# Optimization experiments

Hardware: AMD Instinct MI355X
Metric: run time of the kernel (lower is better)

Reference implementation:

```python
import jax, jax.numpy as jnp
import numpy as np

PATCH = 16
FMAP = 14  # 224 // 16, feature-map / mask resolution
BLUR_K = np.array([[1., 2., 1.], [2., 4., 2.], [1., 2., 1.]], dtype=np.float32) / 16.0  # pascal(3), normalized


def _conv(x, w, stride, pad):
    return jax.lax.conv_general_dilated(
        x, w, (stride, stride), [(pad, pad), (pad, pad)],
        dimension_numbers=("NCHW", "OIHW", "NCHW"))


def _max_blur_pool(x):
    # MaxBlurPool2D(kernel_size=3, stride=2, max_pool_size=2, ceil_mode=False):
    x = jax.lax.reduce_window(x, -jnp.inf, jax.lax.max,
                              (1, 1, 2, 2), (1, 1, 1, 1), "VALID")
    C = x.shape[1]
    kw = jnp.broadcast_to(jnp.asarray(BLUR_K, x.dtype), (C, 1, 3, 3))
    return jax.lax.conv_general_dilated(
        x, kw, (2, 2), [(1, 1), (1, 1)],
        dimension_numbers=("NCHW", "OIHW", "NCHW"), feature_group_count=C)


def _up(m, hw):
    # upsample [B,1,FMAP,FMAP] mask to spatial size hw via repeat_interleave
    f = hw // FMAP
    return jnp.repeat(jnp.repeat(m, f, axis=2), f, axis=3)


def reference(x, masks, w1, w2):
    B = x.shape[0]
    m = masks.reshape(B, 1, FMAP, FMAP).astype(x.dtype)  # fmap-level active mask
    x = x * _up(m, x.shape[2])                 # _apply_masks: zero masked 16x16 patches
    x = _conv(x, w1, 2, 3)                     # B,64,112,112
    x = jax.nn.relu(x * _up(m, x.shape[2]))    # SparK-style sparse conv: re-mask output
    x = _max_blur_pool(x)                      # B,64,56,56
    x = _conv(x, w2, 2, 3)                     # B,768,28,28
    x = jax.nn.relu(x * _up(m, x.shape[2]))    # re-mask output of second sparse conv
    x = _max_blur_pool(x)                      # B,768,14,14
    B_, C, H, W = x.shape
    return x.reshape(B_, C, H * W).transpose(0, 2, 1)  # b (h w) c -> [B,196,768]


def setup_inputs() -> dict:
    key = jax.random.key(0)
    k1, k2, k3, k4 = jax.random.split(key, 4)
    x = jax.random.normal(k1, (64, 3, 224, 224), jnp.float32)
    masks = jax.random.randint(k2, (64, 196), 0, 2).astype(bool)
    # kaiming_normal fan_in scaling as in init_weight
    w1 = jax.random.normal(k3, (64, 3, 7, 7), jnp.float32) * np.float32(np.sqrt(2.0 / (3 * 49)))
    w2 = jax.random.normal(k4, (768, 64, 7, 7), jnp.float32) * np.float32(np.sqrt(2.0 / (64 * 49)))
    return {"x": x, "masks": masks, "w1": w1, "w2": w2}
```

## Files before the change

kernel.cpp:

```cpp
#include <hip/hip_runtime.h>
#include <stdint.h>

typedef __attribute__((ext_vector_type(8))) short short8;
typedef __attribute__((ext_vector_type(4))) float f32x4;

#define DEVFN static __device__ __forceinline__

DEVFN float bf2f(uint16_t u) { union { uint32_t i; float f; } v; v.i = ((uint32_t)u) << 16; return v.f; }
DEVFN uint16_t f2bf(float f) {
  union { float f; uint32_t i; } v; v.f = f;
  uint32_t u = v.i;
  u += 0x7fffu + ((u >> 16) & 1u);
  return (uint16_t)(u >> 16);
}
DEVFN int imin(int a, int b) { return a < b ? a : b; }

DEVFN void gl_lds16(const void* g, void* l) {
  __builtin_amdgcn_global_load_lds(
      (__attribute__((address_space(1))) void*)(void*)g,
      (__attribute__((address_space(3))) void*)l, 16, 0, 0);
}

DEVFN f32x4 mfma16(short8 a, short8 b, f32x4 c) {
  return __builtin_amdgcn_mfma_f32_16x16x32_bf16(a, b, c, 0, 0, 0);
}

static constexpr size_t OFF_XP   = 0;
static constexpr size_t OFF_W1T  = 27557888;
static constexpr size_t OFF_W2T  = 27586560;
static constexpr size_t OFF_Y1   = 32403456;
static constexpr size_t OFF_P1   = 135163904;
static constexpr size_t OFF_Y2   = 166653952;
static constexpr size_t OFF_LIST = 243724288;
static constexpr size_t OFF_CNT  = 243774464;
static constexpr size_t WS_NEED  = 243774664;

__global__ __launch_bounds__(256) void k_count(const int* __restrict__ masks, int* __restrict__ cnts) {
  int b = blockIdx.x;
  int gid = b * 256 + threadIdx.x;
  unsigned long long m = __ballot(masks[gid] != 0);
  __shared__ int wsum[4];
  if ((threadIdx.x & 63) == 0) wsum[threadIdx.x >> 6] = __popcll(m);
  __syncthreads();
  if (threadIdx.x == 0) cnts[b] = wsum[0] + wsum[1] + wsum[2] + wsum[3];
}

__global__ __launch_bounds__(256) void k_emit(const int* __restrict__ masks, const int* __restrict__ cnts,
                                              int* __restrict__ list, int* __restrict__ total) {
  int b = blockIdx.x;
  int gid = b * 256 + threadIdx.x;
  int lane = threadIdx.x & 63, wave = threadIdx.x >> 6;
  int base = 0;
  for (int i = 0; i < b; ++i) base += cnts[i];
  bool f = masks[gid] != 0;
  unsigned long long m = __ballot(f);
  __shared__ int wcnt[4];
  if (lane == 0) wcnt[wave] = __popcll(m);
  __syncthreads();
  int woff = 0;
  for (int i = 0; i < wave; ++i) woff += wcnt[i];
  if (f) list[base + woff + __popcll(m & ((1ull << lane) - 1ull))] = gid;
  if (b == 48 && threadIdx.x == 0)
    *total = base + wcnt[0] + wcnt[1] + wcnt[2] + wcnt[3];
}

__global__ __launch_bounds__(256) void k_prep(const float* __restrict__ x, const int* __restrict__ masks,
                                              uint16_t* __restrict__ xp) {
  int gid = blockIdx.x * 256 + threadIdx.x;
  int b = gid / 53824;
  int rc = gid - b * 53824;
  int r2 = rc / 232;
  int c2 = rc - r2 * 232;
  int r = r2 - 3, c = c2 - 3;
  uint16_t o0 = 0, o1 = 0, o2 = 0;
  if ((unsigned)r < 224u && (unsigned)c < 224u) {
    if (masks[b * 196 + (r >> 4) * 14 + (c >> 4)]) {
      const float* px = x + (((size_t)b * 3) * 224 + r) * 224 + c;
      o0 = f2bf(px[0]);
      o1 = f2bf(px[50176]);
      o2 = f2bf(px[100352]);
    }
  }
  ushort4 o; o.x = o0; o.y = o1; o.z = o2; o.w = 0;
  *(ushort4*)(xp + (size_t)gid * 4) = o;
}

__global__ __launch_bounds__(256) void k_wt(const float* __restrict__ w1, const float* __restrict__ w2,
                                            uint16_t* __restrict__ w1t, uint16_t* __restrict__ w2t) {
  int gid = blockIdx.x * 256 + threadIdx.x;
  if (gid < 14336) {
    int kh = gid / 2048; int r = gid - kh * 2048;
    int oc = r >> 5, slot = r & 31;
    int kw = slot >> 2, ic = slot & 3;
    float v = 0.f;
    if (kw < 7 && ic < 3) v = w1[((oc * 3 + ic) * 7 + kh) * 7 + kw];
    w1t[gid] = f2bf(v);
  } else {
    int g2 = gid - 14336;
    int khw = g2 / 49152; int r = g2 - khw * 49152;
    int oc = r >> 6, ic = r & 63;
    int kh = khw / 7, kw = khw - kh * 7;
    w2t[g2] = f2bf(w2[((oc * 64 + ic) * 7 + kh) * 7 + kw]);
  }
}

__global__ __launch_bounds__(256, 3) void k_conv1(const uint16_t* __restrict__ xp, const uint16_t* __restrict__ w1t,
                                                  const int* __restrict__ list, const int* __restrict__ count,
                                                  uint16_t* __restrict__ y1) {
  __shared__ uint16_t sB[7 * 64 * 32];
  __shared__ int sc[2];

  int cnt = *count;
  int blk = blockIdx.x;
  if (blk * 2 >= cnt) return;
  int tid = threadIdx.x, lane = tid & 63, wave = tid >> 6;
  int csw = (lane & 3) ^ ((lane >> 2) & 3);

  {
    const char* wg = (const char*)w1t;
    char* wl = (char*)sB;
#pragma unroll
    for (int t = 0; t < 7; ++t) {
      int ldsoff = t * 4096 + wave * 1024;
      int goff = t * 4096 + (wave * 16 + (lane >> 2)) * 64 + csw * 16;
      gl_lds16(wg + goff, wl + ldsoff);
    }
  }
  if (tid < 2) sc[tid] = list[imin(blk * 2 + tid, cnt - 1)];
  __syncthreads();

  int wm = wave * 32, mrow = lane & 15, kg = lane >> 4;

  const uint16_t* baseA[2];
#pragma unroll
  for (int i = 0; i < 2; ++i) {
    int row = wm + 16 * i + mrow;
    int cell = sc[row >> 6];
    int b = cell / 196, cc = cell - b * 196;
    int ci = cc / 14, cj = cc - ci * 14;
    int p = row & 63;
    int oh = ci * 8 + (p >> 3), ow = cj * 8 + (p & 7);
    baseA[i] = xp + (((size_t)(b * 232 + 2 * oh)) * 232 + 2 * ow) * 4 + kg * 8;
  }
  int ksw = (kg ^ (mrow & 3)) * 8;

  f32x4 acc[2][4];
#pragma unroll
  for (int i = 0; i < 2; ++i)
#pragma unroll
    for (int j = 0; j < 4; ++j) acc[i][j] = f32x4{0.f, 0.f, 0.f, 0.f};

#pragma unroll
  for (int kh = 0; kh < 7; ++kh) {
    short8 a0 = *(const short8*)(baseA[0] + kh * 928);
    short8 a1 = *(const short8*)(baseA[1] + kh * 928);
    const uint16_t* Bk = sB + kh * 2048;
#pragma unroll
    for (int j = 0; j < 4; ++j) {
      short8 bj = *(const short8*)(Bk + (16 * j + mrow) * 32 + ksw);
      acc[0][j] = mfma16(a0, bj, acc[0][j]);
      acc[1][j] = mfma16(a1, bj, acc[1][j]);
    }
  }

#pragma unroll
  for (int i = 0; i < 2; ++i) {
    int rbase = wm + 16 * i;
    int cellidx = blk * 2 + (rbase >> 6);
    if (cellidx >= cnt) continue;
    int cell = sc[rbase >> 6];
    int b = cell / 196, cc = cell - b * 196;
    int ci = cc / 14, cj = cc - ci * 14;
#pragma unroll
    for (int j = 0; j < 4; ++j) {
      int oc = 16 * j + mrow;
#pragma unroll
      for (int r = 0; r < 4; ++r) {
        int row = rbase + kg * 4 + r;
        int p = row & 63;
        int oh = ci * 8 + (p >> 3), ow = cj * 8 + (p & 7);
        float v = acc[i][j][r];
        v = v > 0.f ? v : 0.f;
        y1[(((size_t)(b * 112 + oh)) * 112 + ow) * 64 + oc] = f2bf(v);
      }
    }
  }
}

__global__ __launch_bounds__(256) void k_pool1(const uint16_t* __restrict__ y1, const int* __restrict__ masks,
                                               uint16_t* __restrict__ p1) {
  __shared__ uint16_t sY[18 * 18 * 64];
  int b = blockIdx.y;
  int tile = blockIdx.x;
  int tr = tile >> 3, tc = tile & 7;
  int pr0 = tr * 8, pc0 = tc * 8;
  int R0 = 2 * pr0 - 7, C0 = 2 * pc0 - 7;
  int tid = threadIdx.x;
  const int* mb = masks + b * 196;

  for (int idx = tid; idx < 2592; idx += 256) {
    int pix = idx >> 3, ch = idx & 7;
    int pr = pix / 18, pc = pix - pr * 18;
    int r = R0 + pr, c = C0 + pc;
    short8 v = {0, 0, 0, 0, 0, 0, 0, 0};
    if ((unsigned)r < 112u && (unsigned)c < 112u && mb[(r >> 3) * 14 + (c >> 3)])
      v = *(const short8*)(y1 + (((size_t)(b * 112 + r)) * 112 + c) * 64 + ch * 8);
    *(short8*)(sY + ((size_t)(pr * 18 + pc)) * 64 + ch * 8) = v;
  }
  __syncthreads();

  for (int it = tid; it < 512; it += 256) {
    int opix = it >> 3, ch = it & 7;
    int lr = opix >> 3, lc = opix & 7;
    int pr = pr0 + lr, pc = pc0 + lc;
    if (pr >= 62 || pc >= 62) continue;
    int oh = pr - 3, ow = pc - 3;
    float acc[8] = {0.f, 0.f, 0.f, 0.f, 0.f, 0.f, 0.f, 0.f};
    if ((unsigned)oh < 56u && (unsigned)ow < 56u) {
      float hm_prev[3][8];
#pragma unroll
      for (int dd = 0; dd < 4; ++dd) {
        float yv[4][8];
        const uint16_t* src = sY + ((size_t)((2 * lr + dd) * 18 + 2 * lc)) * 64 + ch * 8;
#pragma unroll
        for (int e = 0; e < 4; ++e) {
          short8 t8 = *(const short8*)(src + e * 64);
#pragma unroll
          for (int k = 0; k < 8; ++k) yv[e][k] = bf2f((uint16_t)t8[k]);
        }
        float hm[3][8];
#pragma unroll
        for (int e = 0; e < 3; ++e) {
          int qc = 2 * ow - 1 + e;
          float cv = ((unsigned)qc <= 110u) ? 1.f : 0.f;
#pragma unroll
          for (int k = 0; k < 8; ++k) hm[e][k] = cv * fmaxf(yv[e][k], yv[e + 1][k]);
        }
        if (dd > 0) {
          int d = dd - 1;
          int qr = 2 * oh - 1 + d;
          if ((unsigned)qr <= 110u) {
            float wd = (d == 1) ? 2.f : 1.f;
#pragma unroll
            for (int e = 0; e < 3; ++e) {
              float w = wd * ((e == 1) ? 2.f : 1.f);
#pragma unroll
              for (int k = 0; k < 8; ++k) acc[k] += w * fmaxf(hm_prev[e][k], hm[e][k]);
            }
          }
        }
#pragma unroll
        for (int e = 0; e < 3; ++e)
#pragma unroll
          for (int k = 0; k < 8; ++k) hm_prev[e][k] = hm[e][k];
      }
#pragma unroll
      for (int k = 0; k < 8; ++k) acc[k] *= (1.f / 16.f);
    }
    short8 o;
#pragma unroll
    for (int k = 0; k < 8; ++k) o[k] = (short)f2bf(acc[k]);
    *(short8*)(p1 + (((size_t)(b * 62 + pr)) * 62 + pc) * 64 + ch * 8) = o;
  }
}

__global__ __launch_bounds__(256, 3) void k_conv2(const uint16_t* __restrict__ p1, const uint16_t* __restrict__ w2t,
                                                  const int* __restrict__ list, const int* __restrict__ count,
                                                  uint16_t* __restrict__ y2) {
  __shared__ uint16_t sA[128 * 64];
  __shared__ uint16_t sBt[128 * 64];
  __shared__ int scs[32];

  int cnt = *count;
  int gx = blockIdx.x;
  int xcd = gx & 7, s = gx >> 3;
  int y = s % 6, mtl = s / 6;
  int mt = xcd + 8 * mtl;
  if (mt * 32 >= cnt) return;
  int ocb = y * 128;
  int tid = threadIdx.x, lane = tid & 63, wave = tid >> 6;
  int csw = (lane & 7) ^ ((lane >> 3) & 7);

  if (tid < 32) scs[tid] = list[imin(mt * 32 + tid, cnt - 1)];
  __syncthreads();

  int qm = wave & 1, qn = wave >> 1;
  int mrow = lane & 15, kg = lane >> 4;

  const char* gA[4];
#pragma unroll
  for (int t = 0; t < 4; ++t) {
    int r = wave * 32 + t * 8 + (lane >> 3);
    int cell = scs[r >> 2];
    int b = cell / 196, cc = cell - b * 196;
    int ci = cc / 14, cj = cc - ci * 14;
    int p = r & 3;
    int oh = 2 * ci + (p >> 1), ow = 2 * cj + (p & 1);
    gA[t] = (const char*)p1 + (((size_t)(b * 62 + 2 * oh)) * 62 + 2 * ow) * 128 + csw * 16;
  }
  const char* gB[4];
#pragma unroll
  for (int t = 0; t < 4; ++t) {
    int oc = ocb + wave * 32 + t * 8 + (lane >> 3);
    gB[t] = (const char*)w2t + (size_t)oc * 128 + csw * 16;
  }

  f32x4 acc[4][4];
#pragma unroll
  for (int i = 0; i < 4; ++i)
#pragma unroll
    for (int j = 0; j < 4; ++j) acc[i][j] = f32x4{0.f, 0.f, 0.f, 0.f};

  int sw8 = mrow & 7;
  int kh = 0, kw = 0;
  char* la = (char*)sA + wave * 4096;
  char* lb = (char*)sBt + wave * 4096;
  int k0 = (kg ^ sw8) * 8;
  int k1 = ((4 + kg) ^ sw8) * 8;

#pragma unroll 1
  for (int it = 0; it < 49; ++it) {
    size_t offA = (size_t)(kh * 62 + kw) * 128;
    size_t offB = (size_t)it * 98304;
#pragma unroll
    for (int t = 0; t < 4; ++t) gl_lds16(gA[t] + offA, la + t * 1024);
#pragma unroll
    for (int t = 0; t < 4; ++t) gl_lds16(gB[t] + offB, lb + t * 1024);
    __syncthreads();
    short8 a0[4], b0[4], a1[4], b1[4];
#pragma unroll
    for (int i = 0; i < 4; ++i)
      a0[i] = *(const short8*)(sA + (qm * 64 + 16 * i + mrow) * 64 + k0);
#pragma unroll
    for (int j = 0; j < 4; ++j)
      b0[j] = *(const short8*)(sBt + (qn * 64 + 16 * j + mrow) * 64 + k0);
#pragma unroll
    for (int i = 0; i < 4; ++i)
      a1[i] = *(const short8*)(sA + (qm * 64 + 16 * i + mrow) * 64 + k1);
#pragma unroll
    for (int j = 0; j < 4; ++j)
      b1[j] = *(const short8*)(sBt + (qn * 64 + 16 * j + mrow) * 64 + k1);
    __builtin_amdgcn_sched_barrier(0);
    __builtin_amdgcn_s_setprio(1);
#pragma unroll
    for (int i = 0; i < 4; ++i)
#pragma unroll
      for (int j = 0; j < 4; ++j)
        acc[i][j] = mfma16(a0[i], b0[j], acc[i][j]);
    __builtin_amdgcn_s_setprio(0);
    __builtin_amdgcn_sched_barrier(0);
    __builtin_amdgcn_s_setprio(1);
#pragma unroll
    for (int i = 0; i < 4; ++i)
#pragma unroll
      for (int j = 0; j < 4; ++j)
        acc[i][j] = mfma16(a1[i], b1[j], acc[i][j]);
    __builtin_amdgcn_s_setprio(0);
    __syncthreads();
    if (++kw == 7) { kw = 0; ++kh; }
  }

#pragma unroll
  for (int i = 0; i < 4; ++i) {
    int cellslot = qm * 16 + 4 * i + kg;
    int cellidx = mt * 32 + cellslot;
    if (cellidx >= cnt) continue;
    int cell = scs[cellslot];
    int b = cell / 196, cc = cell - b * 196;
    int ci = cc / 14, cj = cc - ci * 14;
#pragma unroll
    for (int j = 0; j < 4; ++j) {
      int oc = ocb + qn * 64 + 16 * j + mrow;
#pragma unroll
      for (int r = 0; r < 4; ++r) {
        int oh = 2 * ci + (r >> 1), ow = 2 * cj + (r & 1);
        float v = acc[i][j][r];
        v = v > 0.f ? v : 0.f;
        y2[(((size_t)(b * 784)) + oh * 28 + ow) * 768 + oc] = f2bf(v);
      }
    }
  }
}

__global__ __launch_bounds__(256) void k_pool2(const uint16_t* __restrict__ y2, const int* __restrict__ masks,
                                               float* __restrict__ out) {
  __shared__ uint16_t sY[4 * 28 * 128];
  int chunk = blockIdx.x, pi = blockIdx.y, b = blockIdx.z;
  int ch0 = chunk * 128;
  int tid = threadIdx.x;
  const int* mb = masks + b * 196;

  for (int idx = tid; idx < 1792; idx += 256) {
    int rc = idx >> 4;
    int sub = idx & 15;
    int k = rc / 28, c = rc - k * 28;
    int r = 2 * pi - 1 + k;
    short8 v = {0, 0, 0, 0, 0, 0, 0, 0};
    if ((unsigned)r < 28u && mb[(r >> 1) * 14 + (c >> 1)])
      v = *(const short8*)(y2 + (((size_t)(b * 784)) + r * 28 + c) * 768 + ch0 + sub * 8);
    *(short8*)(sY + ((size_t)(k * 28 + c)) * 128 + sub * 8) = v;
  }
  __syncthreads();

  for (int idx = tid; idx < 1792; idx += 256) {
    int pj = idx >> 7, ch = idx & 127;
    float v[4][4];
#pragma unroll
    for (int e = 0; e < 4; ++e) {
      int col = 2 * pj - 1 + e;
      bool cv = (unsigned)col < 28u;
#pragma unroll
      for (int k = 0; k < 4; ++k)
        v[k][e] = cv ? bf2f(sY[((size_t)(k * 28 + col)) * 128 + ch]) : 0.f;
    }
    float acc = 0.f;
#pragma unroll
    for (int d = 0; d < 3; ++d) {
      int q = 2 * pi - 1 + d;
      float gd = ((unsigned)q <= 26u) ? ((d == 1) ? 2.f : 1.f) : 0.f;
      float s = 0.f;
#pragma unroll
      for (int e = 0; e < 3; ++e) {
        int q2 = 2 * pj - 1 + e;
        float ge = ((unsigned)q2 <= 26u) ? ((e == 1) ? 2.f : 1.f) : 0.f;
        float m = fmaxf(fmaxf(v[d][e], v[d + 1][e]), fmaxf(v[d][e + 1], v[d + 1][e + 1]));
        s += ge * m;
      }
      acc += gd * s;
    }
    out[(((size_t)(b * 196)) + pi * 14 + pj) * 768 + ch0 + ch] = acc * (1.f / 16.f);
  }
}

extern "C" void kernel_launch(void* const* d_in, const int* in_sizes, int n_in,
                              void* d_out, int out_size, void* d_ws, size_t ws_size,
                              hipStream_t stream) {
  const float* x     = (const float*)d_in[0];
  const int*   masks = (const int*)d_in[1];
  const float* w1    = (const float*)d_in[2];
  const float* w2    = (const float*)d_in[3];

  char* ws = (char*)d_ws;
  if (ws_size < WS_NEED) return;

  uint16_t* xp  = (uint16_t*)(ws + OFF_XP);
  uint16_t* w1t = (uint16_t*)(ws + OFF_W1T);
  uint16_t* w2t = (uint16_t*)(ws + OFF_W2T);
  uint16_t* y1  = (uint16_t*)(ws + OFF_Y1);
  uint16_t* p1  = (uint16_t*)(ws + OFF_P1);
  uint16_t* y2  = (uint16_t*)(ws + OFF_Y2);
  int* list     = (int*)(ws + OFF_LIST);
  int* cnts     = (int*)(ws + OFF_CNT);
  int* total    = cnts + 49;

  k_count<<<49, 256, 0, stream>>>(masks, cnts);
  k_emit<<<49, 256, 0, stream>>>(masks, cnts, list, total);
  k_prep<<<13456, 256, 0, stream>>>(x, masks, xp);
  k_wt<<<9464, 256, 0, stream>>>(w1, w2, w1t, w2t);
  k_conv1<<<6272, 256, 0, stream>>>(xp, w1t, list, total, y1);
  k_pool1<<<dim3(64, 64), 256, 0, stream>>>(y1, masks, p1);
  k_conv2<<<2352, 256, 0, stream>>>(p1, w2t, list, total, y2);
  k_pool2<<<dim3(6, 14, 64), 256, 0, stream>>>(y2, masks, (float*)d_out);
}
```

Baseline: 364.0 us.

## Double-buffer conv2 LDS tiles to overlap global loads with MFMA

```diff
diff --git a/kernel.cpp b/kernel.cpp
--- a/kernel.cpp
+++ b/kernel.cpp
@@ -264,11 +264,11 @@
   }
 }
 
-__global__ __launch_bounds__(256, 3) void k_conv2(const uint16_t* __restrict__ p1, const uint16_t* __restrict__ w2t,
+__global__ __launch_bounds__(256, 2) void k_conv2(const uint16_t* __restrict__ p1, const uint16_t* __restrict__ w2t,
                                                   const int* __restrict__ list, const int* __restrict__ count,
                                                   uint16_t* __restrict__ y2) {
-  __shared__ uint16_t sA[128 * 64];
-  __shared__ uint16_t sBt[128 * 64];
+  __shared__ uint16_t sA[2][128 * 64];
+  __shared__ uint16_t sBt[2][128 * 64];
   __shared__ int scs[32];
 
   int cnt = *count;
@@ -312,34 +312,47 @@
     for (int j = 0; j < 4; ++j) acc[i][j] = f32x4{0.f, 0.f, 0.f, 0.f};
 
   int sw8 = mrow & 7;
-  int kh = 0, kw = 0;
-  char* la = (char*)sA + wave * 4096;
-  char* lb = (char*)sBt + wave * 4096;
   int k0 = (kg ^ sw8) * 8;
   int k1 = ((4 + kg) ^ sw8) * 8;
+  int aoff = (qm * 64 + mrow) * 64;
+  int boff = (qn * 64 + mrow) * 64;
+
+  char* laA[2] = { (char*)sA[0] + wave * 4096, (char*)sA[1] + wave * 4096 };
+  char* laB[2] = { (char*)sBt[0] + wave * 4096, (char*)sBt[1] + wave * 4096 };
+
+#pragma unroll
+  for (int t = 0; t < 4; ++t) gl_lds16(gA[t], laA[0] + t * 1024);
+#pragma unroll
+  for (int t = 0; t < 4; ++t) gl_lds16(gB[t] + 0, laB[0] + t * 1024);
+  __syncthreads();
+
+  int kwn = 1, khn = 0;
+  int cur = 0;
 
 #pragma unroll 1
   for (int it = 0; it < 49; ++it) {
-    size_t offA = (size_t)(kh * 62 + kw) * 128;
-    size_t offB = (size_t)it * 98304;
-#pragma unroll
-    for (int t = 0; t < 4; ++t) gl_lds16(gA[t] + offA, la + t * 1024);
-#pragma unroll
-    for (int t = 0; t < 4; ++t) gl_lds16(gB[t] + offB, lb + t * 1024);
-    __syncthreads();
+    if (it < 48) {
+      size_t offA = (size_t)(khn * 62 + kwn) * 128;
+      size_t offB = (size_t)(it + 1) * 98304;
+      char* la = laA[cur ^ 1];
+      char* lb = laB[cur ^ 1];
+#pragma unroll
+      for (int t = 0; t < 4; ++t) gl_lds16(gA[t] + offA, la + t * 1024);
+#pragma unroll
+      for (int t = 0; t < 4; ++t) gl_lds16(gB[t] + offB, lb + t * 1024);
+      if (++kwn == 7) { kwn = 0; ++khn; }
+    }
+    const uint16_t* cA = sA[cur];
+    const uint16_t* cB = sBt[cur];
     short8 a0[4], b0[4], a1[4], b1[4];
 #pragma unroll
-    for (int i = 0; i < 4; ++i)
-      a0[i] = *(const short8*)(sA + (qm * 64 + 16 * i + mrow) * 64 + k0);
-#pragma unroll
-    for (int j = 0; j < 4; ++j)
-      b0[j] = *(const short8*)(sBt + (qn * 64 + 16 * j + mrow) * 64 + k0);
-#pragma unroll
-    for (int i = 0; i < 4; ++i)
-      a1[i] = *(const short8*)(sA + (qm * 64 + 16 * i + mrow) * 64 + k1);
-#pragma unroll
-    for (int j = 0; j < 4; ++j)
-      b1[j] = *(const short8*)(sBt + (qn * 64 + 16 * j + mrow) * 64 + k1);
+    for (int i = 0; i < 4; ++i) a0[i] = *(const short8*)(cA + aoff + 1024 * i + k0);
+#pragma unroll
+    for (int j = 0; j < 4; ++j) b0[j] = *(const short8*)(cB + boff + 1024 * j + k0);
+#pragma unroll
+    for (int i = 0; i < 4; ++i) a1[i] = *(const short8*)(cA + aoff + 1024 * i + k1);
+#pragma unroll
+    for (int j = 0; j < 4; ++j) b1[j] = *(const short8*)(cB + boff + 1024 * j + k1);
     __builtin_amdgcn_sched_barrier(0);
     __builtin_amdgcn_s_setprio(1);
 #pragma unroll
@@ -356,8 +369,12 @@
       for (int j = 0; j < 4; ++j)
         acc[i][j] = mfma16(a1[i], b1[j], acc[i][j]);
     __builtin_amdgcn_s_setprio(0);
-    __syncthreads();
-    if (++kw == 7) { kw = 0; ++kh; }
+    __builtin_amdgcn_sched_barrier(0);
+    asm volatile("s_waitcnt vmcnt(0)" ::: "memory");
+    __builtin_amdgcn_sched_barrier(0);
+    __builtin_amdgcn_s_barrier();
+    __builtin_amdgcn_sched_barrier(0);
+    cur ^= 1;
   }
 
 #pragma unroll
```

New measurement: 375.2 us. 1.03x slower.

## Fuse front-end prep kernels into one launch and vectorize pool2 epilogue

Applied to the files above, without the earlier changes.

```diff
diff --git a/kernel.cpp b/kernel.cpp
--- a/kernel.cpp
+++ b/kernel.cpp
@@ -35,72 +35,70 @@
 static constexpr size_t OFF_CNT  = 243774464;
 static constexpr size_t WS_NEED  = 243774664;
 
-__global__ __launch_bounds__(256) void k_count(const int* __restrict__ masks, int* __restrict__ cnts) {
-  int b = blockIdx.x;
-  int gid = b * 256 + threadIdx.x;
-  unsigned long long m = __ballot(masks[gid] != 0);
-  __shared__ int wsum[4];
-  if ((threadIdx.x & 63) == 0) wsum[threadIdx.x >> 6] = __popcll(m);
-  __syncthreads();
-  if (threadIdx.x == 0) cnts[b] = wsum[0] + wsum[1] + wsum[2] + wsum[3];
-}
-
-__global__ __launch_bounds__(256) void k_emit(const int* __restrict__ masks, const int* __restrict__ cnts,
-                                              int* __restrict__ list, int* __restrict__ total) {
-  int b = blockIdx.x;
-  int gid = b * 256 + threadIdx.x;
-  int lane = threadIdx.x & 63, wave = threadIdx.x >> 6;
-  int base = 0;
-  for (int i = 0; i < b; ++i) base += cnts[i];
-  bool f = masks[gid] != 0;
-  unsigned long long m = __ballot(f);
-  __shared__ int wcnt[4];
-  if (lane == 0) wcnt[wave] = __popcll(m);
-  __syncthreads();
-  int woff = 0;
-  for (int i = 0; i < wave; ++i) woff += wcnt[i];
-  if (f) list[base + woff + __popcll(m & ((1ull << lane) - 1ull))] = gid;
-  if (b == 48 && threadIdx.x == 0)
-    *total = base + wcnt[0] + wcnt[1] + wcnt[2] + wcnt[3];
-}
-
-__global__ __launch_bounds__(256) void k_prep(const float* __restrict__ x, const int* __restrict__ masks,
-                                              uint16_t* __restrict__ xp) {
-  int gid = blockIdx.x * 256 + threadIdx.x;
-  int b = gid / 53824;
-  int rc = gid - b * 53824;
-  int r2 = rc / 232;
-  int c2 = rc - r2 * 232;
-  int r = r2 - 3, c = c2 - 3;
-  uint16_t o0 = 0, o1 = 0, o2 = 0;
-  if ((unsigned)r < 224u && (unsigned)c < 224u) {
-    if (masks[b * 196 + (r >> 4) * 14 + (c >> 4)]) {
-      const float* px = x + (((size_t)b * 3) * 224 + r) * 224 + c;
-      o0 = f2bf(px[0]);
-      o1 = f2bf(px[50176]);
-      o2 = f2bf(px[100352]);
-    }
-  }
-  ushort4 o; o.x = o0; o.y = o1; o.z = o2; o.w = 0;
-  *(ushort4*)(xp + (size_t)gid * 4) = o;
-}
-
-__global__ __launch_bounds__(256) void k_wt(const float* __restrict__ w1, const float* __restrict__ w2,
-                                            uint16_t* __restrict__ w1t, uint16_t* __restrict__ w2t) {
-  int gid = blockIdx.x * 256 + threadIdx.x;
-  if (gid < 14336) {
-    int kh = gid / 2048; int r = gid - kh * 2048;
-    int oc = r >> 5, slot = r & 31;
-    int kw = slot >> 2, ic = slot & 3;
-    float v = 0.f;
-    if (kw < 7 && ic < 3) v = w1[((oc * 3 + ic) * 7 + kh) * 7 + kw];
-    w1t[gid] = f2bf(v);
+__global__ __launch_bounds__(256) void k_front(const int* __restrict__ masks, const float* __restrict__ x,
+                                               const float* __restrict__ w1, const float* __restrict__ w2,
+                                               int* __restrict__ list, int* __restrict__ total,
+                                               uint16_t* __restrict__ xp, uint16_t* __restrict__ w1t,
+                                               uint16_t* __restrict__ w2t) {
+  int bid = blockIdx.x;
+  int tid = threadIdx.x;
+  if (bid == 0) {
+    __shared__ int sbase;
+    __shared__ int wc[4];
+    int lane = tid & 63, wave = tid >> 6;
+    if (tid == 0) sbase = 0;
+    __syncthreads();
+#pragma unroll 1
+    for (int r = 0; r < 49; ++r) {
+      int gid = r * 256 + tid;
+      bool f = masks[gid] != 0;
+      unsigned long long m = __ballot(f);
+      if (lane == 0) wc[wave] = __popcll(m);
+      __syncthreads();
+      int b0 = sbase;
+      int woff = 0;
+      for (int i = 0; i < wave; ++i) woff += wc[i];
+      if (f) list[b0 + woff + __popcll(m & ((1ull << lane) - 1ull))] = gid;
+      int rt = wc[0] + wc[1] + wc[2] + wc[3];
+      __syncthreads();
+      if (tid == 0) sbase = b0 + rt;
+    }
+    __syncthreads();
+    if (tid == 0) *total = sbase;
+  } else if (bid <= 13456) {
+    int gid = (bid - 1) * 256 + tid;
+    int b = gid / 53824;
+    int rc = gid - b * 53824;
+    int r2 = rc / 232;
+    int c2 = rc - r2 * 232;
+    int r = r2 - 3, c = c2 - 3;
+    uint16_t o0 = 0, o1 = 0, o2 = 0;
+    if ((unsigned)r < 224u && (unsigned)c < 224u) {
+      if (masks[b * 196 + (r >> 4) * 14 + (c >> 4)]) {
+        const float* px = x + (((size_t)b * 3) * 224 + r) * 224 + c;
+        o0 = f2bf(px[0]);
+        o1 = f2bf(px[50176]);
+        o2 = f2bf(px[100352]);
+      }
+    }
+    ushort4 o; o.x = o0; o.y = o1; o.z = o2; o.w = 0;
+    *(ushort4*)(xp + (size_t)gid * 4) = o;
   } else {
-    int g2 = gid - 14336;
-    int khw = g2 / 49152; int r = g2 - khw * 49152;
-    int oc = r >> 6, ic = r & 63;
-    int kh = khw / 7, kw = khw - kh * 7;
-    w2t[g2] = f2bf(w2[((oc * 64 + ic) * 7 + kh) * 7 + kw]);
+    int gid = (bid - 13457) * 256 + tid;
+    if (gid < 14336) {
+      int kh = gid / 2048; int r = gid - kh * 2048;
+      int oc = r >> 5, slot = r & 31;
+      int kw = slot >> 2, ic = slot & 3;
+      float v = 0.f;
+      if (kw < 7 && ic < 3) v = w1[((oc * 3 + ic) * 7 + kh) * 7 + kw];
+      w1t[gid] = f2bf(v);
+    } else {
+      int g2 = gid - 14336;
+      int khw = g2 / 49152; int r = g2 - khw * 49152;
+      int oc = r >> 6, ic = r & 63;
+      int kh = khw / 7, kw = khw - kh * 7;
+      w2t[g2] = f2bf(w2[((oc * 64 + ic) * 7 + kh) * 7 + kw]);
+    }
   }
 }
 
@@ -402,33 +400,57 @@
   }
   __syncthreads();
 
-  for (int idx = tid; idx < 1792; idx += 256) {
-    int pj = idx >> 7, ch = idx & 127;
-    float v[4][4];
+  if (tid < 224) {
+    int pj = tid >> 4, chg = tid & 15;
+    float gd[3];
+#pragma unroll
+    for (int d = 0; d < 3; ++d) {
+      int q = 2 * pi - 1 + d;
+      gd[d] = ((unsigned)q <= 26u) ? ((d == 1) ? 2.f : 1.f) : 0.f;
+    }
+    float acc[8] = {0.f, 0.f, 0.f, 0.f, 0.f, 0.f, 0.f, 0.f};
+    float pvp[3][8];
 #pragma unroll
     for (int e = 0; e < 4; ++e) {
       int col = 2 * pj - 1 + e;
-      bool cv = (unsigned)col < 28u;
-#pragma unroll
-      for (int k = 0; k < 4; ++k)
-        v[k][e] = cv ? bf2f(sY[((size_t)(k * 28 + col)) * 128 + ch]) : 0.f;
-    }
-    float acc = 0.f;
-#pragma unroll
-    for (int d = 0; d < 3; ++d) {
-      int q = 2 * pi - 1 + d;
-      float gd = ((unsigned)q <= 26u) ? ((d == 1) ? 2.f : 1.f) : 0.f;
-      float s = 0.f;
-#pragma unroll
-      for (int e = 0; e < 3; ++e) {
-        int q2 = 2 * pj - 1 + e;
-        float ge = ((unsigned)q2 <= 26u) ? ((e == 1) ? 2.f : 1.f) : 0.f;
-        float m = fmaxf(fmaxf(v[d][e], v[d + 1][e]), fmaxf(v[d][e + 1], v[d + 1][e + 1]));
-        s += ge * m;
-      }
-      acc += gd * s;
-    }
-    out[(((size_t)(b * 196)) + pi * 14 + pj) * 768 + ch0 + ch] = acc * (1.f / 16.f);
+      float f[4][8];
+      if ((unsigned)col < 28u) {
+#pragma unroll
+        for (int k = 0; k < 4; ++k) {
+          short8 t8 = *(const short8*)(sY + ((size_t)(k * 28 + col)) * 128 + chg * 8);
+#pragma unroll
+          for (int j = 0; j < 8; ++j) f[k][j] = bf2f((uint16_t)t8[j]);
+        }
+      } else {
+#pragma unroll
+        for (int k = 0; k < 4; ++k)
+#pragma unroll
+          for (int j = 0; j < 8; ++j) f[k][j] = 0.f;
+      }
+      float pvc[3][8];
+#pragma unroll
+      for (int d = 0; d < 3; ++d)
+#pragma unroll
+        for (int j = 0; j < 8; ++j) pvc[d][j] = fmaxf(f[d][j], f[d + 1][j]);
+      if (e > 0) {
+        int tap = e - 1;
+        int q2 = 2 * pj - 1 + tap;
+        float ge = ((unsigned)q2 <= 26u) ? ((tap == 1) ? 2.f : 1.f) : 0.f;
+#pragma unroll
+        for (int d = 0; d < 3; ++d) {
+          float w = gd[d] * ge;
+#pragma unroll
+          for (int j = 0; j < 8; ++j) acc[j] += w * fmaxf(pvp[d][j], pvc[d][j]);
+        }
+      }
+#pragma unroll
+      for (int d = 0; d < 3; ++d)
+#pragma unroll
+        for (int j = 0; j < 8; ++j) pvp[d][j] = pvc[d][j];
+    }
+    float* po = out + (((size_t)(b * 196)) + pi * 14 + pj) * 768 + ch0 + chg * 8;
+#pragma unroll
+    for (int j = 0; j < 8; ++j) po[j] = acc[j] * (1.f / 16.f);
   }
 }
 
@@ -453,10 +475,7 @@
   int* cnts     = (int*)(ws + OFF_CNT);
   int* total    = cnts + 49;
 
-  k_count<<<49, 256, 0, stream>>>(masks, cnts);
-  k_emit<<<49, 256, 0, stream>>>(masks, cnts, list, total);
-  k_prep<<<13456, 256, 0, stream>>>(x, masks, xp);
-  k_wt<<<9464, 256, 0, stream>>>(w1, w2, w1t, w2t);
+  k_front<<<22921, 256, 0, stream>>>(masks, x, w1, w2, list, total, xp, w1t, w2t);
   k_conv1<<<6272, 256, 0, stream>>>(xp, w1t, list, total, y1);
   k_pool1<<<dim3(64, 64), 256, 0, stream>>>(y1, masks, p1);
   k_conv2<<<2352, 256, 0, stream>>>(p1, w2t, list, total, y2);
```

New measurement: 353.9 us. -2.8%, faster.
